# Kernel tuning notes

Measured on AMD Instinct MI355X. Metric: run time of the kernel, lower is better.

Reference implementation:

```python
import jax, jax.numpy as jnp
import numpy as np

D0 = 1.0          # constraint distance d
NPEND = 128       # points per pendulum chain
NB = 1024         # number of chains (= batch.max()+1)
LATENT = 256      # latent dim of y
NDIM = 3          # spatial dimensions; x dim = 2*NDIM (pos + vel)


def setup_inputs() -> dict:
    key = jax.random.key(0)
    k1, k2, k3 = jax.random.split(key, 3)
    N = NB * NPEND
    y = jax.random.normal(k1, (N, LATENT), dtype=jnp.float32)
    z = jax.random.normal(k2, (N,), dtype=jnp.float32)
    K = jax.random.normal(k3, (LATENT, 2 * NDIM), dtype=jnp.float32) * 0.05
    batch = (jnp.arange(N, dtype=jnp.int32) // NPEND).astype(jnp.int32)
    return {"y": y, "z": z, "K": K, "batch": batch}


def _delta_r(r):
    # dr[:,0] = r[:,0]; dr[:,i] = r[:,i] - r[:,i-1]
    return jnp.concatenate([r[:, :1], r[:, 1:] - r[:, :-1]], axis=1)


def reference(y, z, K, batch):
    x = y @ K                                  # [N, 6]
    ndim = x.shape[-1] // 2                    # pos_only=False -> 3
    nb = batch.shape[0] // NPEND               # == batch.max()+1 by construction
    r = x[:, :ndim].reshape(nb, -1, ndim)      # [nb, npend, 3]

    dr = _delta_r(r)                           # [nb, npend, 3]
    drnorm = jnp.linalg.norm(dr, axis=-1)      # [nb, npend]
    c = drnorm - D0                            # constraint values
    rn = dr / drnorm[..., None]                # unit chain-difference vectors

    # Jacobian-transpose times constraints, fused over the chain dimension:
    # out[:,i] = c_i * rn_i - c_{i+1} * rn_{i+1};  out[:,-1] = c_{-1} * rn_{-1}
    t = c[..., None] * rn                      # [nb, npend, 3]
    out = t - jnp.concatenate([t[:, 1:], jnp.zeros_like(t[:, :1])], axis=1)

    lam_x = jnp.zeros_like(x).at[:, :ndim].set(out.reshape(-1, ndim))
    lam_y = lam_x @ K.T                        # [N, latent]
    return lam_y
```

## Files before the change

### kernel.cpp

```cpp
#include <hip/hip_runtime.h>

#define NPEND  128
#define LATENT 256
#define KCOLS  6
#define D0_C   1.0f
#define NB_MAX 1024

typedef float f32x4 __attribute__((ext_vector_type(4)));

static __device__ float4 g_r[(size_t)NB_MAX * NPEND];

__global__ __launch_bounds__(256, 4)
void pend_r_kernel(const float* __restrict__ y,
                   const float* __restrict__ K,
                   int ngroups)
{
    const int tid  = threadIdx.x;
    const int lane = tid & 63;
    const int g    = lane >> 4;
    const int sl   = lane & 15;
    const int k0   = sl * 16;

    float kf0[16], kf1[16], kf2[16];
#pragma unroll
    for (int i = 0; i < 16; ++i) {
        kf0[i] = K[(k0 + i) * KCOLS + 0];
        kf1[i] = K[(k0 + i) * KCOLS + 1];
        kf2[i] = K[(k0 + i) * KCOLS + 2];
    }

    const int wid    = (blockIdx.x << 2) | (tid >> 6);
    const int wcount = gridDim.x << 2;

    for (int grp = wid; grp < ngroups; grp += wcount) {
        const int row = (grp << 2) + g;
        const float* yr = y + (size_t)row * LATENT + k0;
        const float4 a0 = *(const float4*)(yr + 0);
        const float4 a1 = *(const float4*)(yr + 4);
        const float4 a2 = *(const float4*)(yr + 8);
        const float4 a3 = *(const float4*)(yr + 12);

        const float av[16] = { a0.x, a0.y, a0.z, a0.w,
                               a1.x, a1.y, a1.z, a1.w,
                               a2.x, a2.y, a2.z, a2.w,
                               a3.x, a3.y, a3.z, a3.w };
        float s0 = 0.f, s1 = 0.f, s2 = 0.f;
#pragma unroll
        for (int i = 0; i < 16; ++i) {
            s0 += av[i] * kf0[i];
            s1 += av[i] * kf1[i];
            s2 += av[i] * kf2[i];
        }

#pragma unroll
        for (int off = 8; off >= 1; off >>= 1) {
            s0 += __shfl_xor(s0, off, 16);
            s1 += __shfl_xor(s1, off, 16);
            s2 += __shfl_xor(s2, off, 16);
        }
        if (sl == 0) g_r[row] = make_float4(s0, s1, s2, 0.f);
    }
}

__global__ __launch_bounds__(256, 8)
void pend_out_kernel(const float* __restrict__ K,
                     float* __restrict__ out)
{
    __shared__ float  sKT[3][LATENT];
    __shared__ float4 sRr[36];

    const int tid  = threadIdx.x;
    const int hwid = tid >> 5;
    const int hl   = tid & 31;
    const int l0   = hl * 4;

    const int chain = blockIdx.x >> 2;
    const int seg   = blockIdx.x & 3;
    const int row0  = seg * 32;
    const int rlo   = (row0 > 0) ? row0 - 1 : 0;
    const int rhi   = (row0 + 32 < NPEND) ? row0 + 32 : NPEND - 1;
    const int nrows = rhi - rlo + 1;

    {
        const float ka = K[tid * KCOLS + 0];
        const float kb = K[tid * KCOLS + 1];
        const float kc = K[tid * KCOLS + 2];
        sKT[0][tid] = ka;
        sKT[1][tid] = kb;
        sKT[2][tid] = kc;
    }
    if (tid < nrows) sRr[tid] = g_r[chain * NPEND + rlo + tid];
    __syncthreads();

    const float4 k0a = *(const float4*)&sKT[0][l0];
    const float4 k0b = *(const float4*)&sKT[0][l0 + 128];
    const float4 k1a = *(const float4*)&sKT[1][l0];
    const float4 k1b = *(const float4*)&sKT[1][l0 + 128];
    const float4 k2a = *(const float4*)&sKT[2][l0];
    const float4 k2b = *(const float4*)&sKT[2][l0 + 128];

    const size_t cbase = (size_t)chain * ((size_t)NPEND * LATENT);

#pragma unroll
    for (int j = 0; j < 4; ++j) {
        const int i   = hwid + 8 * j;
        const int row = row0 + i;
        const int si  = row - rlo;

        const float4 rc = sRr[si];
        const float rx = rc.x, ry = rc.y, rz = rc.z;
        float px = 0.f, py = 0.f, pz = 0.f;
        if (row > 0) { const float4 rp = sRr[si - 1]; px = rp.x; py = rp.y; pz = rp.z; }

        const float dx = rx - px, dy = ry - py, dz = rz - pz;
        const float n  = sqrtf(dx*dx + dy*dy + dz*dz);
        const float s  = (n - D0_C) / n;
        float ox = s * dx, oy = s * dy, oz = s * dz;

        if (row < NPEND - 1) {
            const float4 rn = sRr[si + 1];
            const float ex = rn.x - rx, ey = rn.y - ry, ez = rn.z - rz;
            const float n2 = sqrtf(ex*ex + ey*ey + ez*ez);
            const float t2 = (n2 - D0_C) / n2;
            ox -= t2 * ex; oy -= t2 * ey; oz -= t2 * ez;
        }

        f32x4 wa, wb;
        wa.x = ox*k0a.x + oy*k1a.x + oz*k2a.x;
        wa.y = ox*k0a.y + oy*k1a.y + oz*k2a.y;
        wa.z = ox*k0a.z + oy*k1a.z + oz*k2a.z;
        wa.w = ox*k0a.w + oy*k1a.w + oz*k2a.w;
        wb.x = ox*k0b.x + oy*k1b.x + oz*k2b.x;
        wb.y = ox*k0b.y + oy*k1b.y + oz*k2b.y;
        wb.z = ox*k0b.z + oy*k1b.z + oz*k2b.z;
        wb.w = ox*k0b.w + oy*k1b.w + oz*k2b.w;

        float* orow = out + cbase + (size_t)row * LATENT;
        __builtin_nontemporal_store(wa, (f32x4*)(orow + l0));
        __builtin_nontemporal_store(wb, (f32x4*)(orow + 128 + l0));
    }
}

extern "C" void kernel_launch(void* const* d_in, const int* in_sizes, int n_in,
                              void* d_out, int out_size, void* d_ws, size_t ws_size,
                              hipStream_t stream) {
    const float* y = (const float*)d_in[0];
    const float* K = (const float*)d_in[2];
    float* out = (float*)d_out;

    int N  = (n_in > 1 && in_sizes) ? in_sizes[1] : (1024 * NPEND);
    int nb = N / NPEND;
    if (nb <= 0) nb = 1024;
    if (nb > NB_MAX) nb = NB_MAX;
    N = nb * NPEND;
    (void)out_size; (void)d_ws; (void)ws_size;

    const int ngroups = N / 4;
    pend_r_kernel<<<2048, 256, 0, stream>>>(y, K, ngroups);
    pend_out_kernel<<<nb * 4, 256, 0, stream>>>(K, out);
}
```

Before: 245.8 us.

## Software-pipeline y loads in projection kernel and make output kernel persistent

The projection kernel drops its grid-stride loop for a fixed unroll of four row groups per wave. It keeps two groups of y loads in flight, uses sched_barriers to overlap loads with FMAs, and changes lane indexing so 16 lanes read contiguous 256-byte spans. The output kernel becomes a persistent grid-stride launch that keeps K columns in registers and reads neighbouring r values straight from global memory, removing the LDS staging and the block barrier. Risk: the projection kernel now covers only four groups per wave, so it relies on the fixed problem size to cover every row.

```diff
diff --git a/kernel.cpp b/kernel.cpp
--- a/kernel.cpp
+++ b/kernel.cpp
@@ -19,123 +19,121 @@
     const int lane = tid & 63;
     const int g    = lane >> 4;
     const int sl   = lane & 15;
-    const int k0   = sl * 16;
+
+    const int nwaves = gridDim.x << 2;
+    const int wid    = (blockIdx.x << 2) | (tid >> 6);
+
+    const int g0 = wid;
+    const int g1 = wid + nwaves;
+    const int g2 = wid + 2 * nwaves;
+    const int g3 = wid + 3 * nwaves;
+
+    float4 b0[4], b1[4];
+
+    auto issue = [&](int grp, float4 (&b)[4]) {
+        const float* p = y + (size_t)(grp * 4 + g) * LATENT + sl * 4;
+#pragma unroll
+        for (int j = 0; j < 4; ++j)
+            b[j] = *(const float4*)(p + j * 64);
+    };
+
+    if (g0 < ngroups) issue(g0, b0);
+    if (g1 < ngroups) issue(g1, b1);
 
     float kf0[16], kf1[16], kf2[16];
 #pragma unroll
-    for (int i = 0; i < 16; ++i) {
-        kf0[i] = K[(k0 + i) * KCOLS + 0];
-        kf1[i] = K[(k0 + i) * KCOLS + 1];
-        kf2[i] = K[(k0 + i) * KCOLS + 2];
-    }
+    for (int j = 0; j < 4; ++j)
+#pragma unroll
+        for (int e = 0; e < 4; ++e) {
+            const int k = j * 64 + sl * 4 + e;
+            kf0[4 * j + e] = K[k * KCOLS + 0];
+            kf1[4 * j + e] = K[k * KCOLS + 1];
+            kf2[4 * j + e] = K[k * KCOLS + 2];
+        }
 
-    const int wid    = (blockIdx.x << 2) | (tid >> 6);
-    const int wcount = gridDim.x << 2;
-
-    for (int grp = wid; grp < ngroups; grp += wcount) {
-        const int row = (grp << 2) + g;
-        const float* yr = y + (size_t)row * LATENT + k0;
-        const float4 a0 = *(const float4*)(yr + 0);
-        const float4 a1 = *(const float4*)(yr + 4);
-        const float4 a2 = *(const float4*)(yr + 8);
-        const float4 a3 = *(const float4*)(yr + 12);
-
-        const float av[16] = { a0.x, a0.y, a0.z, a0.w,
-                               a1.x, a1.y, a1.z, a1.w,
-                               a2.x, a2.y, a2.z, a2.w,
-                               a3.x, a3.y, a3.z, a3.w };
+    auto consume = [&](const float4 (&b)[4], int grp) {
         float s0 = 0.f, s1 = 0.f, s2 = 0.f;
 #pragma unroll
-        for (int i = 0; i < 16; ++i) {
-            s0 += av[i] * kf0[i];
-            s1 += av[i] * kf1[i];
-            s2 += av[i] * kf2[i];
+        for (int j = 0; j < 4; ++j) {
+            const float4 a = b[j];
+            s0 += a.x*kf0[4*j] + a.y*kf0[4*j+1] + a.z*kf0[4*j+2] + a.w*kf0[4*j+3];
+            s1 += a.x*kf1[4*j] + a.y*kf1[4*j+1] + a.z*kf1[4*j+2] + a.w*kf1[4*j+3];
+            s2 += a.x*kf2[4*j] + a.y*kf2[4*j+1] + a.z*kf2[4*j+2] + a.w*kf2[4*j+3];
         }
-
 #pragma unroll
         for (int off = 8; off >= 1; off >>= 1) {
             s0 += __shfl_xor(s0, off, 16);
             s1 += __shfl_xor(s1, off, 16);
             s2 += __shfl_xor(s2, off, 16);
         }
-        if (sl == 0) g_r[row] = make_float4(s0, s1, s2, 0.f);
-    }
+        if (sl == 0) g_r[grp * 4 + g] = make_float4(s0, s1, s2, 0.f);
+    };
+
+    __builtin_amdgcn_sched_barrier(0);
+    if (g0 < ngroups) consume(b0, g0);
+    if (g2 < ngroups) issue(g2, b0);
+    __builtin_amdgcn_sched_barrier(0);
+    if (g1 < ngroups) consume(b1, g1);
+    if (g3 < ngroups) issue(g3, b1);
+    __builtin_amdgcn_sched_barrier(0);
+    if (g2 < ngroups) consume(b0, g2);
+    if (g3 < ngroups) consume(b1, g3);
 }
 
-__global__ __launch_bounds__(256, 8)
+__global__ __launch_bounds__(256, 4)
 void pend_out_kernel(const float* __restrict__ K,
-                     float* __restrict__ out)
+                     float* __restrict__ out,
+                     int nrows)
 {
-    __shared__ float  sKT[3][LATENT];
-    __shared__ float4 sRr[36];
+    const int tid = threadIdx.x;
+    const int hl  = tid & 31;
+    const int l0  = hl * 4;
 
-    const int tid  = threadIdx.x;
-    const int hwid = tid >> 5;
-    const int hl   = tid & 31;
-    const int l0   = hl * 4;
+    float ka[8], kb[8], kc[8];
+#pragma unroll
+    for (int e = 0; e < 4; ++e) {
+        ka[e]     = K[(l0 + e) * KCOLS + 0];
+        kb[e]     = K[(l0 + e) * KCOLS + 1];
+        kc[e]     = K[(l0 + e) * KCOLS + 2];
+        ka[4 + e] = K[(l0 + 128 + e) * KCOLS + 0];
+        kb[4 + e] = K[(l0 + 128 + e) * KCOLS + 1];
+        kc[4 + e] = K[(l0 + 128 + e) * KCOLS + 2];
+    }
 
-    const int chain = blockIdx.x >> 2;
-    const int seg   = blockIdx.x & 3;
-    const int row0  = seg * 32;
-    const int rlo   = (row0 > 0) ? row0 - 1 : 0;
-    const int rhi   = (row0 + 32 < NPEND) ? row0 + 32 : NPEND - 1;
-    const int nrows = rhi - rlo + 1;
+    const int hh  = blockIdx.x * 8 + (tid >> 5);
+    const int nhh = gridDim.x * 8;
 
-    {
-        const float ka = K[tid * KCOLS + 0];
-        const float kb = K[tid * KCOLS + 1];
-        const float kc = K[tid * KCOLS + 2];
-        sKT[0][tid] = ka;
-        sKT[1][tid] = kb;
-        sKT[2][tid] = kc;
-    }
-    if (tid < nrows) sRr[tid] = g_r[chain * NPEND + rlo + tid];
-    __syncthreads();
+    for (int row = hh; row < nrows; row += nhh) {
+        const int p = row & (NPEND - 1);
 
-    const float4 k0a = *(const float4*)&sKT[0][l0];
-    const float4 k0b = *(const float4*)&sKT[0][l0 + 128];
-    const float4 k1a = *(const float4*)&sKT[1][l0];
-    const float4 k1b = *(const float4*)&sKT[1][l0 + 128];
-    const float4 k2a = *(const float4*)&sKT[2][l0];
-    const float4 k2b = *(const float4*)&sKT[2][l0 + 128];
+        const float4 rc = g_r[row];
+        float px = 0.f, py = 0.f, pz = 0.f;
+        if (p > 0) { const float4 rp = g_r[row - 1]; px = rp.x; py = rp.y; pz = rp.z; }
 
-    const size_t cbase = (size_t)chain * ((size_t)NPEND * LATENT);
-
-#pragma unroll
-    for (int j = 0; j < 4; ++j) {
-        const int i   = hwid + 8 * j;
-        const int row = row0 + i;
-        const int si  = row - rlo;
-
-        const float4 rc = sRr[si];
-        const float rx = rc.x, ry = rc.y, rz = rc.z;
-        float px = 0.f, py = 0.f, pz = 0.f;
-        if (row > 0) { const float4 rp = sRr[si - 1]; px = rp.x; py = rp.y; pz = rp.z; }
-
-        const float dx = rx - px, dy = ry - py, dz = rz - pz;
+        const float dx = rc.x - px, dy = rc.y - py, dz = rc.z - pz;
         const float n  = sqrtf(dx*dx + dy*dy + dz*dz);
         const float s  = (n - D0_C) / n;
         float ox = s * dx, oy = s * dy, oz = s * dz;
 
-        if (row < NPEND - 1) {
-            const float4 rn = sRr[si + 1];
-            const float ex = rn.x - rx, ey = rn.y - ry, ez = rn.z - rz;
+        if (p < NPEND - 1) {
+            const float4 rn = g_r[row + 1];
+            const float ex = rn.x - rc.x, ey = rn.y - rc.y, ez = rn.z - rc.z;
             const float n2 = sqrtf(ex*ex + ey*ey + ez*ez);
             const float t2 = (n2 - D0_C) / n2;
             ox -= t2 * ex; oy -= t2 * ey; oz -= t2 * ez;
         }
 
         f32x4 wa, wb;
-        wa.x = ox*k0a.x + oy*k1a.x + oz*k2a.x;
-        wa.y = ox*k0a.y + oy*k1a.y + oz*k2a.y;
-        wa.z = ox*k0a.z + oy*k1a.z + oz*k2a.z;
-        wa.w = ox*k0a.w + oy*k1a.w + oz*k2a.w;
-        wb.x = ox*k0b.x + oy*k1b.x + oz*k2b.x;
-        wb.y = ox*k0b.y + oy*k1b.y + oz*k2b.y;
-        wb.z = ox*k0b.z + oy*k1b.z + oz*k2b.z;
-        wb.w = ox*k0b.w + oy*k1b.w + oz*k2b.w;
+        wa.x = ox*ka[0] + oy*kb[0] + oz*kc[0];
+        wa.y = ox*ka[1] + oy*kb[1] + oz*kc[1];
+        wa.z = ox*ka[2] + oy*kb[2] + oz*kc[2];
+        wa.w = ox*ka[3] + oy*kb[3] + oz*kc[3];
+        wb.x = ox*ka[4] + oy*kb[4] + oz*kc[4];
+        wb.y = ox*ka[5] + oy*kb[5] + oz*kc[5];
+        wb.z = ox*ka[6] + oy*kb[6] + oz*kc[6];
+        wb.w = ox*ka[7] + oy*kb[7] + oz*kc[7];
 
-        float* orow = out + cbase + (size_t)row * LATENT;
+        float* orow = out + (size_t)row * LATENT;
         __builtin_nontemporal_store(wa, (f32x4*)(orow + l0));
         __builtin_nontemporal_store(wb, (f32x4*)(orow + 128 + l0));
     }
@@ -157,5 +155,5 @@
 
     const int ngroups = N / 4;
     pend_r_kernel<<<2048, 256, 0, stream>>>(y, K, ngroups);
-    pend_out_kernel<<<nb * 4, 256, 0, stream>>>(K, out);
+    pend_out_kernel<<<2048, 256, 0, stream>>>(K, out, N);
 }
```

Result: faster. 238.2 us (-3.1%).
